# Performance work log

Measured on AMD Instinct MI355X. Metric: run time of the kernel, lower is better.

The kernel has to match this reference:

```python
import jax, jax.numpy as jnp
import numpy as np

B, S, D = 1, 2048, 3072
H, DH = 24, 128
ENC, NIP = 512, 64
COND = (512 // 8) * (512 // 8) * 16 // 64  # 1024 cond tokens per lora
RANK, ALPHA, LW, IP_SCALE = 16, 16.0, 1.0, 1.0
EPS = 1e-5


def _rms(x):
    return x * jax.lax.rsqrt(jnp.mean(x * x, axis=-1, keepdims=True) + EPS)


def _to_heads(x):
    b, s, _ = x.shape
    return x.reshape(b, s, H, DH).transpose(0, 2, 1, 3)  # [B,H,S,DH]


def _from_heads(x):
    b, h, s, d = x.shape
    return x.transpose(0, 2, 1, 3).reshape(b, s, h * d)


def _lora(x, dn, up):
    # token mask keeps only the cond block (number=0, n_loras=1 -> last COND tokens)
    y = ((x[:, -COND:, :] @ dn) @ up) * (ALPHA / RANK)
    z = jnp.zeros((x.shape[0], x.shape[1] - COND, up.shape[1]), x.dtype)
    return jnp.concatenate([z, y], axis=1)


def _sdpa(q, k, v, mask=None):
    s = jnp.einsum('bhqd,bhkd->bhqk', q, k) * (1.0 / np.sqrt(DH))
    if mask is not None:
        s = s + mask
    return jnp.einsum('bhqk,bhkd->bhqd', jax.nn.softmax(s, axis=-1), v)


def _forward(hidden_states, encoder_hidden_states, image_emb,
             Wq, bq, Wk, bk, Wv, bv, Waq, baq, Wak, bak, Wav, bav,
             Wo, bo, Wao, bao, Wkip, Wvip,
             lq_dn, lq_up, lk_dn, lk_up, lv_dn, lv_up, lp_dn, lp_up):
    hs, ehs, img = hidden_states, encoder_hidden_states, image_emb
    # context (encoder) projections + RMSNorm on q/k
    eq = _rms(_to_heads(ehs @ Waq + baq))
    ek = _rms(_to_heads(ehs @ Wak + bak))
    ev = _to_heads(ehs @ Wav + bav)
    # main-stream q/k/v with masked LoRA branches
    q = hs @ Wq + bq + LW * _lora(hs, lq_dn, lq_up)
    k = hs @ Wk + bk + LW * _lora(hs, lk_dn, lk_up)
    v = hs @ Wv + bv + LW * _lora(hs, lv_dn, lv_up)
    q = _rms(_to_heads(q))
    k = _rms(_to_heads(k))
    v = _to_heads(v)
    # IP-adapter branch: extra K/V from image_emb, norm_added_k is RMSNorm(128)
    kip = _rms(_to_heads(img @ Wkip))
    vip = _to_heads(img @ Wvip)
    ip_out = _from_heads(_sdpa(q, kip, vip))  # [B,S,D]
    # concat encoder stream ahead of main stream
    q = jnp.concatenate([eq, q], axis=2)
    k = jnp.concatenate([ek, k], axis=2)
    v = jnp.concatenate([ev, v], axis=2)
    SL = ENC + S
    SB = SL - COND  # scaled_block_size
    m = jnp.ones((SL, SL), jnp.float32)
    m = m.at[:SB, :].set(0.0)        # non-cond rows attend everywhere
    m = m.at[SB:, SB:].set(0.0)      # single cond block attends to itself (n_loras=1)
    mask = m * (-1e20)
    out = _from_heads(_sdpa(q, k, v, mask))  # [B,SL,D]
    enc_out = out[:, :ENC, :]
    main = out[:, ENC:, :] + IP_SCALE * ip_out
    main = main @ Wo + bo
    main = main + LW * _lora(main, lp_dn, lp_up)  # proj LoRA (to_out dropout=identity)
    enc_out = enc_out @ Wao + bao
    return jnp.concatenate([enc_out, main], axis=1)  # [B, ENC+S, D]


def setup_inputs():
    key = jax.random.key(0)
    ks = iter(jax.random.split(key, 40))
    w = lambda *sh: jax.random.normal(next(ks), sh, jnp.float32) * 0.02
    return dict(
        hidden_states=jax.random.normal(next(ks), (B, S, D), jnp.float32),
        encoder_hidden_states=jax.random.normal(next(ks), (B, ENC, D), jnp.float32),
        image_emb=jax.random.normal(next(ks), (B, NIP, D), jnp.float32),
        Wq=w(D, D), bq=w(D), Wk=w(D, D), bk=w(D), Wv=w(D, D), bv=w(D),
        Waq=w(D, D), baq=w(D), Wak=w(D, D), bak=w(D), Wav=w(D, D), bav=w(D),
        Wo=w(D, D), bo=w(D), Wao=w(D, D), bao=w(D),
        Wkip=w(D, D), Wvip=w(D, D),
        lq_dn=w(D, RANK), lq_up=w(RANK, D), lk_dn=w(D, RANK), lk_up=w(RANK, D),
        lv_dn=w(D, RANK), lv_up=w(RANK, D), lp_dn=w(D, RANK), lp_up=w(RANK, D),
    )


def reference(hidden_states, encoder_hidden_states, image_emb,
              Wq, bq, Wk, bk, Wv, bv, Waq, baq, Wak, bak, Wav, bav,
              Wo, bo, Wao, bao, Wkip, Wvip,
              lq_dn, lq_up, lk_dn, lk_up, lv_dn, lv_up, lp_dn, lp_up):
    return _forward(hidden_states, encoder_hidden_states, image_emb,
                    Wq, bq, Wk, bk, Wv, bv, Waq, baq, Wak, bak, Wav, bav,
                    Wo, bo, Wao, bao, Wkip, Wvip,
                    lq_dn, lq_up, lk_dn, lk_up, lv_dn, lv_up, lp_dn, lp_up)
```

## Files before the change

kernel.cpp:

```cpp
#include <hip/hip_runtime.h>

typedef unsigned short u16;
typedef short s16x8 __attribute__((ext_vector_type(8)));
typedef float f32x4 __attribute__((ext_vector_type(4)));
typedef const __attribute__((address_space(1))) unsigned int* as1_u32p;
typedef __attribute__((address_space(3))) unsigned int* as3_u32p;

static_assert(sizeof(s16x8) == 16, "");

struct alignas(8) U16x4 { u16 x, y, z, w; };

__device__ __forceinline__ u16 f2bf(float f) {
  union { float f; unsigned u; } c; c.f = f;
  return (u16)((c.u + 0x7fffu + ((c.u >> 16) & 1u)) >> 16);
}
__device__ __forceinline__ float bf2f(u16 h) {
  union { unsigned u; float f; } c; c.u = ((unsigned)h) << 16;
  return c.f;
}
__device__ __forceinline__ void async16(const void* g, void* l) {
  __builtin_amdgcn_global_load_lds((as1_u32p)g, (as3_u32p)l, 16, 0, 0);
}

__launch_bounds__(256)
__global__ void cvt_bf16(const float* __restrict__ in, u16* __restrict__ out, long n) {
  long i = ((long)blockIdx.x * 256 + threadIdx.x) * 8;
  if (i >= n) return;
  float4 a = *(const float4*)(in + i);
  float4 b = *(const float4*)(in + i + 4);
  U16x4 o0{f2bf(a.x), f2bf(a.y), f2bf(a.z), f2bf(a.w)};
  U16x4 o1{f2bf(b.x), f2bf(b.y), f2bf(b.z), f2bf(b.w)};
  *(U16x4*)(out + i) = o0;
  *(U16x4*)(out + i + 4) = o1;
}

__launch_bounds__(256)
__global__ void cvt_hs(const float* __restrict__ hs, const float* __restrict__ tl,
                       u16* __restrict__ hsb) {
  long idx = (long)blockIdx.x * 256 + threadIdx.x;
  long m = idx / 392, c = idx % 392;
  U16x4 o0, o1;
  if (c < 384) {
    const float* p = hs + m * 3072 + c * 8;
    float4 a = *(const float4*)p;
    float4 b = *(const float4*)(p + 4);
    o0 = U16x4{f2bf(a.x), f2bf(a.y), f2bf(a.z), f2bf(a.w)};
    o1 = U16x4{f2bf(b.x), f2bf(b.y), f2bf(b.z), f2bf(b.w)};
  } else {
    u16 t[8];
#pragma unroll
    for (int i = 0; i < 8; ++i) {
      int r = (int)(c - 384) * 8 + i;
      float v = (m >= 1024 && r < 48) ? tl[(m - 1024) * 48 + r] : 0.f;
      t[i] = f2bf(v);
    }
    o0 = U16x4{t[0], t[1], t[2], t[3]};
    o1 = U16x4{t[4], t[5], t[6], t[7]};
  }
  u16* d = hsb + m * 3136 + c * 8;
  *(U16x4*)d = o0;
  *(U16x4*)(d + 4) = o1;
}

__launch_bounds__(256)
__global__ void pack_bias(const float* __restrict__ a, const float* __restrict__ b,
                          const float* __restrict__ c, float* __restrict__ out) {
  int i = blockIdx.x * 256 + threadIdx.x;
  if (i >= 9216) return;
  out[i] = (i < 3072) ? a[i] : (i < 6144) ? b[i - 3072] : c[i - 6144];
}

struct WTArgs { const float* src[3]; u16* dst[3]; };

__launch_bounds__(256)
__global__ void transpose_w(WTArgs args, int ldd) {
  const float* src = args.src[blockIdx.z];
  u16* dst = args.dst[blockIdx.z];
  __shared__ float tile[32][33];
  int k0 = blockIdx.x * 32, n0 = blockIdx.y * 32;
  int r = threadIdx.x >> 3, c4 = (threadIdx.x & 7) * 4;
  float4 v = *(const float4*)(src + (long)(k0 + r) * 3072 + n0 + c4);
  tile[r][c4 + 0] = v.x; tile[r][c4 + 1] = v.y;
  tile[r][c4 + 2] = v.z; tile[r][c4 + 3] = v.w;
  __syncthreads();
  U16x4 o{f2bf(tile[c4 + 0][r]), f2bf(tile[c4 + 1][r]),
          f2bf(tile[c4 + 2][r]), f2bf(tile[c4 + 3][r])};
  *(U16x4*)(dst + (long)(n0 + r) * ldd + k0 + c4) = o;
}

__launch_bounds__(256)
__global__ void fill_wtail(const float* __restrict__ u0, const float* __restrict__ u1,
                           const float* __restrict__ u2, u16* __restrict__ WTb) {
  int idx = blockIdx.x * 256 + threadIdx.x;
  int n = idx >> 6, i = idx & 63;
  int seg = n / 3072;
  const float* up = (seg == 0) ? u0 : (seg == 1) ? u1 : u2;
  int r = i - seg * 16;
  float v = (r >= 0 && r < 16) ? up[(long)r * 3072 + (n - seg * 3072)] : 0.f;
  WTb[(long)n * 3136 + 3072 + i] = f2bf(v);
}

__launch_bounds__(256)
__global__ void transpose_v(const u16* __restrict__ VB, u16* __restrict__ VT, int T) {
  __shared__ u16 tile[32][34];
  int h = blockIdx.z;
  int t0 = blockIdx.x * 32, d0 = blockIdx.y * 32;
  int r = threadIdx.x >> 3, c4 = (threadIdx.x & 7) * 4;
  U16x4 v = *(const U16x4*)(VB + ((long)h * T + t0 + r) * 128 + d0 + c4);
  tile[r][c4 + 0] = v.x; tile[r][c4 + 1] = v.y;
  tile[r][c4 + 2] = v.z; tile[r][c4 + 3] = v.w;
  __syncthreads();
  U16x4 o{tile[c4 + 0][r], tile[c4 + 1][r], tile[c4 + 2][r], tile[c4 + 3][r]};
  *(U16x4*)(VT + ((long)h * 128 + d0 + r) * T + t0 + c4) = o;
}

__launch_bounds__(256)
__global__ void rms_heads4(const float* __restrict__ in, int col0,
                           u16* __restrict__ out, int do_rms) {
  const int t = blockIdx.x;
  const int w = threadIdx.x >> 6, lane = threadIdx.x & 63;
  const long ps = 64LL * 6144;
#pragma unroll
  for (int hh = 0; hh < 6; ++hh) {
    int h = w * 6 + hh;
    const float* x = in + (long)t * 6144 + col0 + h * 128 + lane * 2;
    float a = x[0] + x[ps] + x[2 * ps] + x[3 * ps];
    float b = x[1] + x[1 + ps] + x[1 + 2 * ps] + x[1 + 3 * ps];
    float scale = 1.f;
    if (do_rms) {
      float ss = a * a + b * b;
#pragma unroll
      for (int st = 1; st < 64; st <<= 1) ss += __shfl_xor(ss, st, 64);
      scale = rsqrtf(ss * (1.f / 128.f) + 1e-5f);
    }
    unsigned pa = f2bf(a * scale), pb = f2bf(b * scale);
    *(unsigned*)(out + ((long)h * 64 + t) * 128 + lane * 2) = pa | (pb << 16);
  }
}

__launch_bounds__(256)
__global__ void lora_dn3(const float* __restrict__ X, int ldx,
                         const float* __restrict__ d0, const float* __restrict__ d1,
                         const float* __restrict__ d2, float* __restrict__ t) {
  __shared__ float red[4][48];
  const int m = blockIdx.x;
  const float* xr = X + (long)m * ldx;
  float p[48];
#pragma unroll
  for (int r = 0; r < 48; ++r) p[r] = 0.f;
  for (int k = threadIdx.x; k < 3072; k += 256) {
    float a = xr[k];
    const float* e0 = d0 + (long)k * 16;
    const float* e1 = d1 + (long)k * 16;
    const float* e2 = d2 + (long)k * 16;
#pragma unroll
    for (int r = 0; r < 16; ++r) {
      p[r]      += a * e0[r];
      p[16 + r] += a * e1[r];
      p[32 + r] += a * e2[r];
    }
  }
#pragma unroll
  for (int r = 0; r < 48; ++r)
#pragma unroll
    for (int st = 1; st < 64; st <<= 1) p[r] += __shfl_xor(p[r], st, 64);
  int lane = threadIdx.x & 63, w = threadIdx.x >> 6;
  if (lane == 0) {
#pragma unroll
    for (int r = 0; r < 48; ++r) red[w][r] = p[r];
  }
  __syncthreads();
  if (threadIdx.x < 48) {
    int r = threadIdx.x;
    t[(long)m * 48 + r] = red[0][r] + red[1][r] + red[2][r] + red[3][r];
  }
}

__launch_bounds__(256)
__global__ void lora_dn(const float* __restrict__ X, int ldx,
                        const float* __restrict__ dn, float* __restrict__ t) {
  __shared__ float red[4][16];
  const int m = blockIdx.x;
  const float* xr = X + (long)m * ldx;
  float p[16];
#pragma unroll
  for (int r = 0; r < 16; ++r) p[r] = 0.f;
  for (int k = threadIdx.x; k < 3072; k += 256) {
    float a = xr[k];
    const float* d = dn + (long)k * 16;
#pragma unroll
    for (int r = 0; r < 16; ++r) p[r] += a * d[r];
  }
#pragma unroll
  for (int r = 0; r < 16; ++r)
#pragma unroll
    for (int st = 1; st < 64; st <<= 1) p[r] += __shfl_xor(p[r], st, 64);
  int lane = threadIdx.x & 63, w = threadIdx.x >> 6;
  if (lane == 0) {
#pragma unroll
    for (int r = 0; r < 16; ++r) red[w][r] = p[r];
  }
  __syncthreads();
  if (threadIdx.x < 16) {
    int r = threadIdx.x;
    t[(long)m * 16 + r] = red[0][r] + red[1][r] + red[2][r] + red[3][r];
  }
}

__launch_bounds__(256)
__global__ void lora_up(const float* __restrict__ t, const float* __restrict__ up,
                        float* __restrict__ Y, int ldy) {
  const int m = blockIdx.x;
  float tv[16];
#pragma unroll
  for (int r = 0; r < 16; ++r) tv[r] = t[(long)m * 16 + r];
  float* yr = Y + (long)m * ldy;
  for (int n = threadIdx.x; n < 3072; n += 256) {
    float a = 0.f;
#pragma unroll
    for (int r = 0; r < 16; ++r) a += tv[r] * up[(long)r * 3072 + n];
    yr[n] += a;
  }
}

template <int BM, int MI, int NI>
__launch_bounds__(256)
__global__ void gemm_f32(const u16* __restrict__ A, int lda,
                         const u16* __restrict__ B, int ldb,
                         float* __restrict__ C, int ldc,
                         const float* __restrict__ bias, int KC, long cstride) {
  constexpr int WCOLS = 128 / (NI * 16);
  constexpr int ABYTES = BM * 128;
  __shared__ char smem[ABYTES + 128 * 128];
  char* As = smem;
  char* Bs = smem + ABYTES;
  const int tid = threadIdx.x;
  const int w = tid >> 6, lane = tid & 63;
  const int lr = lane & 15, lg = lane >> 4;
  const int wr = w / WCOLS, wc = w % WCOLS;
  const int nbx = gridDim.x;
  const int nwg = nbx * gridDim.y;
  const int flat = blockIdx.y * nbx + blockIdx.x;
  const int swz = (flat & 7) * (nwg >> 3) + (flat >> 3);
  const long m0 = (long)(swz % nbx) * BM;
  const long n0 = (long)(swz / nbx) * 128;
  const int k0 = blockIdx.z * KC;
  C += blockIdx.z * cstride;
  f32x4 acc[MI][NI] = {};
  constexpr int ACH = BM / 32;
  for (int kb = k0; kb < k0 + KC; kb += 64) {
    __syncthreads();
#pragma unroll
    for (int i = 0; i < ACH; ++i) {
      int x = (tid + 256 * i) * 16;
      int row = x >> 7;
      int sx = x ^ ((row & 7) << 4);
      async16((const char*)(A + (m0 + row) * lda + kb) + (sx & 127),
              As + ((w << 10) + (i << 12)));
    }
#pragma unroll
    for (int i = 0; i < 4; ++i) {
      int x = (tid + 256 * i) * 16;
      int row = x >> 7;
      int sx = x ^ ((row & 7) << 4);
      async16((const char*)(B + (n0 + row) * ldb + kb) + (sx & 127),
              Bs + ((w << 10) + (i << 12)));
    }
    __syncthreads();
#pragma unroll
    for (int kc = 0; kc < 2; ++kc) {
      s16x8 af[MI], bfr[NI];
#pragma unroll
      for (int mi = 0; mi < MI; ++mi) {
        int row = wr * (MI * 16) + mi * 16 + lr;
        int b = ((row << 7) + kc * 64 + lg * 16) ^ ((row & 7) << 4);
        af[mi] = *(const s16x8*)(As + b);
      }
#pragma unroll
      for (int ni = 0; ni < NI; ++ni) {
        int row = wc * (NI * 16) + ni * 16 + lr;
        int b = ((row << 7) + kc * 64 + lg * 16) ^ ((row & 7) << 4);
        bfr[ni] = *(const s16x8*)(Bs + b);
      }
#pragma unroll
      for (int mi = 0; mi < MI; ++mi)
#pragma unroll
        for (int ni = 0; ni < NI; ++ni)
          acc[mi][ni] = __builtin_amdgcn_mfma_f32_16x16x32_bf16(af[mi], bfr[ni], acc[mi][ni], 0, 0, 0);
    }
  }
#pragma unroll
  for (int mi = 0; mi < MI; ++mi) {
#pragma unroll
    for (int ni = 0; ni < NI; ++ni) {
      long col = n0 + wc * (NI * 16) + ni * 16 + lr;
      float bv = bias ? bias[col] : 0.f;
#pragma unroll
      for (int j = 0; j < 4; ++j) {
        long row = m0 + wr * (MI * 16) + mi * 16 + lg * 4 + j;
        C[row * ldc + col] = acc[mi][ni][j] + bv;
      }
    }
  }
}

__launch_bounds__(256)
__global__ void gemm_qkv(const u16* __restrict__ A, int lda,
                         const u16* __restrict__ B, int ldb,
                         u16* __restrict__ Qo, u16* __restrict__ Ko, u16* __restrict__ VTo,
                         int t0, const float* __restrict__ bias, int K) {
  __shared__ char smem[128 * 128 + 128 * 128];
  char* As = smem;
  char* Bs = smem + 128 * 128;
  const int tid = threadIdx.x;
  const int w = tid >> 6, lane = tid & 63;
  const int lr = lane & 15, lg = lane >> 4;
  const int wr = w >> 1, wc = w & 1;
  const int nbx = gridDim.x;
  const int nwg = nbx * gridDim.y;
  const int flat = blockIdx.y * nbx + blockIdx.x;
  const int swz = (flat & 7) * (nwg >> 3) + (flat >> 3);
  const long m0 = (long)(swz % nbx) * 128;
  const long n0 = (long)(swz / nbx) * 128;
  f32x4 acc[4][4] = {};
  for (int kb = 0; kb < K; kb += 64) {
    __syncthreads();
#pragma unroll
    for (int i = 0; i < 4; ++i) {
      int x = (tid + 256 * i) * 16;
      int row = x >> 7;
      int sx = x ^ ((row & 7) << 4);
      async16((const char*)(A + (m0 + row) * lda + kb) + (sx & 127),
              As + ((w << 10) + (i << 12)));
    }
#pragma unroll
    for (int i = 0; i < 4; ++i) {
      int x = (tid + 256 * i) * 16;
      int row = x >> 7;
      int sx = x ^ ((row & 7) << 4);
      async16((const char*)(B + (n0 + row) * ldb + kb) + (sx & 127),
              Bs + ((w << 10) + (i << 12)));
    }
    __syncthreads();
#pragma unroll
    for (int kc = 0; kc < 2; ++kc) {
      s16x8 af[4], bfr[4];
#pragma unroll
      for (int mi = 0; mi < 4; ++mi) {
        int row = wr * 64 + mi * 16 + lr;
        int b = ((row << 7) + kc * 64 + lg * 16) ^ ((row & 7) << 4);
        af[mi] = *(const s16x8*)(As + b);
      }
#pragma unroll
      for (int ni = 0; ni < 4; ++ni) {
        int row = wc * 64 + ni * 16 + lr;
        int b = ((row << 7) + kc * 64 + lg * 16) ^ ((row & 7) << 4);
        bfr[ni] = *(const s16x8*)(Bs + b);
      }
#pragma unroll
      for (int mi = 0; mi < 4; ++mi)
#pragma unroll
        for (int ni = 0; ni < 4; ++ni)
          acc[mi][ni] = __builtin_amdgcn_mfma_f32_16x16x32_bf16(af[mi], bfr[ni], acc[mi][ni], 0, 0, 0);
    }
  }
  const int seg = (int)(n0 / 3072);
  const int head = (int)((n0 % 3072) >> 7);
#pragma unroll
  for (int ni = 0; ni < 4; ++ni) {
    float bv = bias[n0 + wc * 64 + ni * 16 + lr];
#pragma unroll
    for (int mi = 0; mi < 4; ++mi)
#pragma unroll
      for (int j = 0; j < 4; ++j) acc[mi][ni][j] += bv;
  }
  if (seg < 2) {
    u16* out = (seg == 0) ? Qo : Ko;
    float scl[4][4];
#pragma unroll
    for (int mi = 0; mi < 4; ++mi)
#pragma unroll
      for (int j = 0; j < 4; ++j) {
        float s = 0.f;
#pragma unroll
        for (int ni = 0; ni < 4; ++ni) s += acc[mi][ni][j] * acc[mi][ni][j];
#pragma unroll
        for (int st = 1; st < 16; st <<= 1) s += __shfl_xor(s, st, 16);
        scl[mi][j] = s;
      }
    __syncthreads();
    float* red = (float*)smem;
    if (lr == 0) {
#pragma unroll
      for (int mi = 0; mi < 4; ++mi)
#pragma unroll
        for (int j = 0; j < 4; ++j)
          red[((((wr * 4 + mi) * 4 + lg) * 4 + j) << 1) + wc] = scl[mi][j];
    }
    __syncthreads();
#pragma unroll
    for (int mi = 0; mi < 4; ++mi)
#pragma unroll
      for (int j = 0; j < 4; ++j) {
        int ix = (((wr * 4 + mi) * 4 + lg) * 4 + j) << 1;
        float t = red[ix] + red[ix + 1];
        scl[mi][j] = rsqrtf(t * (1.f / 128.f) + 1e-5f);
      }
#pragma unroll
    for (int mi = 0; mi < 4; ++mi)
#pragma unroll
      for (int ni = 0; ni < 4; ++ni) {
        int d = wc * 64 + ni * 16 + lr;
#pragma unroll
        for (int j = 0; j < 4; ++j) {
          long tok = t0 + m0 + wr * 64 + mi * 16 + lg * 4 + j;
          out[((long)head * 2560 + tok) * 128 + d] = f2bf(acc[mi][ni][j] * scl[mi][j]);
        }
      }
  } else {
#pragma unroll
    for (int mi = 0; mi < 4; ++mi)
#pragma unroll
      for (int ni = 0; ni < 4; ++ni) {
        long tok0 = t0 + m0 + wr * 64 + mi * 16 + lg * 4;
        int d = wc * 64 + ni * 16 + lr;
        U16x4 o{f2bf(acc[mi][ni][0]), f2bf(acc[mi][ni][1]),
                f2bf(acc[mi][ni][2]), f2bf(acc[mi][ni][3])};
        *(U16x4*)(VTo + ((long)head * 128 + d) * 2560 + tok0) = o;
      }
  }
}

__launch_bounds__(256)
__global__ void gemm_out(const u16* __restrict__ Atok, const u16* __restrict__ WT,
                         float* __restrict__ outp, const float* __restrict__ bao,
                         const float* __restrict__ bo) {
  __shared__ char smem[128 * 128 + 128 * 128];
  char* As = smem;
  char* Bs = smem + 128 * 128;
  const int tid = threadIdx.x;
  const int w = tid >> 6, lane = tid & 63;
  const int lr = lane & 15, lg = lane >> 4;
  const int wr = w >> 1, wc = w & 1;
  const int flat = blockIdx.y * 20 + blockIdx.x;
  const int swz = (flat & 7) * 60 + (flat >> 3);
  const int mx = swz % 20;
  const long n0 = (long)(swz / 20) * 128;
  const u16* A;
  const u16* B;
  const float* bias;
  float* C;
  long m0;
  if (mx < 4) { A = Atok; B = WT; bias = bao; C = outp; m0 = (long)mx * 128; }
  else { A = Atok + 512L * 3072; B = WT + 3072L * 3136; bias = bo; C = outp + 512L * 3072; m0 = (long)(mx - 4) * 128; }
  f32x4 acc[4][4] = {};
  for (int kb = 0; kb < 3072; kb += 64) {
    __syncthreads();
#pragma unroll
    for (int i = 0; i < 4; ++i) {
      int x = (tid + 256 * i) * 16;
      int row = x >> 7;
      int sx = x ^ ((row & 7) << 4);
      async16((const char*)(A + (m0 + row) * 3072 + kb) + (sx & 127),
              As + ((w << 10) + (i << 12)));
    }
#pragma unroll
    for (int i = 0; i < 4; ++i) {
      int x = (tid + 256 * i) * 16;
      int row = x >> 7;
      int sx = x ^ ((row & 7) << 4);
      async16((const char*)(B + (n0 + row) * 3136 + kb) + (sx & 127),
              Bs + ((w << 10) + (i << 12)));
    }
    __syncthreads();
#pragma unroll
    for (int kc = 0; kc < 2; ++kc) {
      s16x8 af[4], bfr[4];
#pragma unroll
      for (int mi = 0; mi < 4; ++mi) {
        int row = wr * 64 + mi * 16 + lr;
        int b = ((row << 7) + kc * 64 + lg * 16) ^ ((row & 7) << 4);
        af[mi] = *(const s16x8*)(As + b);
      }
#pragma unroll
      for (int ni = 0; ni < 4; ++ni) {
        int row = wc * 64 + ni * 16 + lr;
        int b = ((row << 7) + kc * 64 + lg * 16) ^ ((row & 7) << 4);
        bfr[ni] = *(const s16x8*)(Bs + b);
      }
#pragma unroll
      for (int mi = 0; mi < 4; ++mi)
#pragma unroll
        for (int ni = 0; ni < 4; ++ni)
          acc[mi][ni] = __builtin_amdgcn_mfma_f32_16x16x32_bf16(af[mi], bfr[ni], acc[mi][ni], 0, 0, 0);
    }
  }
#pragma unroll
  for (int mi = 0; mi < 4; ++mi) {
#pragma unroll
    for (int ni = 0; ni < 4; ++ni) {
      long col = n0 + wc * 64 + ni * 16 + lr;
      float bv = bias[col];
#pragma unroll
      for (int j = 0; j < 4; ++j) {
        long row = m0 + wr * 64 + mi * 16 + lg * 4 + j;
        C[row * 3072 + col] = acc[mi][ni][j] + bv;
      }
    }
  }
}

__launch_bounds__(512, 4)
__global__ void attn_fused(const u16* __restrict__ QB, const u16* __restrict__ KB,
                           const u16* __restrict__ VT, const u16* __restrict__ KipB,
                           const u16* __restrict__ VipT, u16* __restrict__ OutTok) {
  __shared__ char smem[81920];
  const int tid = threadIdx.x, w = tid >> 6, lane = tid & 63;
  const int lr = lane & 15, lg = lane >> 4;
  const int h = blockIdx.y;
  const int q0 = blockIdx.x * 128;
  const bool ip = (q0 >= 512);
  const u16* Qrow = QB + (long)(h * 2560 + q0 + w * 16 + lr) * 128;
  s16x8 qf[4];
#pragma unroll
  for (int dc = 0; dc < 4; ++dc) qf[dc] = *(const s16x8*)(Qrow + dc * 32 + lg * 8);
  f32x4 accO[8] = {};
  float l_r[4] = {0.f, 0.f, 0.f, 0.f};
  const int kv0 = (q0 >= 1536) ? 1536 : 0;
  const float sc = 0.08838834764831845f;

  auto stage_main = [&](int kv, int buf) {
#pragma unroll
    for (int i = 0; i < 2; ++i) {
      int x = (tid + 512 * i) * 16;
      int row = x >> 8;
      int sx = x ^ ((row & 7) << 4);
      async16((const char*)(KB + (long)(h * 2560 + kv + row) * 128) + (sx & 255),
              smem + buf * 16384 + ((i << 13) + (w << 10)));
    }
#pragma unroll
    for (int i = 0; i < 2; ++i) {
      int x = (tid + 512 * i) * 16;
      int row = x >> 7;
      int sx = x ^ ((row & 7) << 4);
      async16((const char*)(VT + (long)(h * 128 + row) * 2560 + kv) + (sx & 127),
              smem + 32768 + buf * 16384 + ((i << 13) + (w << 10)));
    }
  };
  auto stage_ip = [&](int buf) {
#pragma unroll
    for (int i = 0; i < 2; ++i) {
      int x = (tid + 512 * i) * 16;
      int row = x >> 8;
      int sx = x ^ ((row & 7) << 4);
      async16((const char*)(KipB + (long)(h * 64 + row) * 128) + (sx & 255),
              smem + buf * 16384 + ((i << 13) + (w << 10)));
    }
#pragma unroll
    for (int i = 0; i < 2; ++i) {
      int x = (tid + 512 * i) * 16;
      int row = x >> 7;
      int sx = x ^ ((row & 7) << 4);
      async16((const char*)(VipT + (long)(h * 128 + row) * 64) + (sx & 127),
              smem + 32768 + buf * 16384 + ((i << 13) + (w << 10)));
    }
  };

  stage_main(kv0, 0);
  __syncthreads();
  int cur = 0;
  for (int kv = kv0; kv < 2560; kv += 64) {
    if (kv + 64 < 2560) stage_main(kv + 64, cur ^ 1);
    else if (ip) stage_ip(cur ^ 1);
    const char* Ks = smem + cur * 16384;
    const char* Vs = smem + 32768 + cur * 16384;
    char* Pw = smem + 65536 + w * 2048;
    f32x4 s[4] = {};
#pragma unroll
    for (int kt = 0; kt < 4; ++kt)
#pragma unroll
      for (int dc = 0; dc < 4; ++dc) {
        int row = kt * 16 + lr;
        int b = ((row << 8) + dc * 64 + lg * 16) ^ ((row & 7) << 4);
        s16x8 kf = *(const s16x8*)(Ks + b);
        s[kt] = __builtin_amdgcn_mfma_f32_16x16x32_bf16(qf[dc], kf, s[kt], 0, 0, 0);
      }
#pragma unroll
    for (int kt = 0; kt < 4; ++kt)
#pragma unroll
      for (int j = 0; j < 4; ++j) {
        float pv = __expf(fmaf(s[kt][j], sc, -12.0f));
        l_r[j] += pv;
        int prow = lg * 4 + j;
        int b = ((prow << 7) + (kt * 16 + lr) * 2) ^ ((prow & 7) << 4);
        *(u16*)(Pw + b) = f2bf(pv);
      }
    asm volatile("s_waitcnt lgkmcnt(0)" ::: "memory");
#pragma unroll
    for (int kc = 0; kc < 2; ++kc) {
      int pb = ((lr << 7) + kc * 64 + lg * 16) ^ ((lr & 7) << 4);
      s16x8 pf = *(const s16x8*)(Pw + pb);
#pragma unroll
      for (int dt = 0; dt < 8; ++dt) {
        int row = dt * 16 + lr;
        int b = ((row << 7) + kc * 64 + lg * 16) ^ ((row & 7) << 4);
        s16x8 vf = *(const s16x8*)(Vs + b);
        accO[dt] = __builtin_amdgcn_mfma_f32_16x16x32_bf16(pf, vf, accO[dt], 0, 0, 0);
      }
    }
    __syncthreads();
    cur ^= 1;
  }
#pragma unroll
  for (int j = 0; j < 4; ++j) {
#pragma unroll
    for (int st = 1; st < 16; st <<= 1) l_r[j] += __shfl_xor(l_r[j], st, 16);
    l_r[j] = 1.f / l_r[j];
  }
#pragma unroll
  for (int dt = 0; dt < 8; ++dt)
#pragma unroll
    for (int j = 0; j < 4; ++j) accO[dt][j] *= l_r[j];
  if (ip) {
    const char* Ks = smem + cur * 16384;
    const char* Vs = smem + 32768 + cur * 16384;
    char* Pw = smem + 65536 + w * 2048;
    f32x4 s2[4] = {};
#pragma unroll
    for (int kt = 0; kt < 4; ++kt)
#pragma unroll
      for (int dc = 0; dc < 4; ++dc) {
        int row = kt * 16 + lr;
        int b = ((row << 8) + dc * 64 + lg * 16) ^ ((row & 7) << 4);
        s16x8 kf = *(const s16x8*)(Ks + b);
        s2[kt] = __builtin_amdgcn_mfma_f32_16x16x32_bf16(qf[dc], kf, s2[kt], 0, 0, 0);
      }
    float p2[4][4];
    float l2[4] = {0.f, 0.f, 0.f, 0.f};
#pragma unroll
    for (int kt = 0; kt < 4; ++kt)
#pragma unroll
      for (int j = 0; j < 4; ++j) {
        float pv = __expf(fmaf(s2[kt][j], sc, -12.0f));
        p2[kt][j] = pv;
        l2[j] += pv;
      }
#pragma unroll
    for (int j = 0; j < 4; ++j) {
#pragma unroll
      for (int st = 1; st < 16; st <<= 1) l2[j] += __shfl_xor(l2[j], st, 16);
      l2[j] = 1.f / l2[j];
    }
#pragma unroll
    for (int kt = 0; kt < 4; ++kt)
#pragma unroll
      for (int j = 0; j < 4; ++j) {
        int prow = lg * 4 + j;
        int b = ((prow << 7) + (kt * 16 + lr) * 2) ^ ((prow & 7) << 4);
        *(u16*)(Pw + b) = f2bf(p2[kt][j] * l2[j]);
      }
    asm volatile("s_waitcnt lgkmcnt(0)" ::: "memory");
#pragma unroll
    for (int kc = 0; kc < 2; ++kc) {
      int pb = ((lr << 7) + kc * 64 + lg * 16) ^ ((lr & 7) << 4);
      s16x8 pf = *(const s16x8*)(Pw + pb);
#pragma unroll
      for (int dt = 0; dt < 8; ++dt) {
        int row = dt * 16 + lr;
        int b = ((row << 7) + kc * 64 + lg * 16) ^ ((row & 7) << 4);
        s16x8 vf = *(const s16x8*)(Vs + b);
        accO[dt] = __builtin_amdgcn_mfma_f32_16x16x32_bf16(pf, vf, accO[dt], 0, 0, 0);
      }
    }
  }
#pragma unroll
  for (int j = 0; j < 4; ++j) {
    long tok = q0 + w * 16 + lg * 4 + j;
#pragma unroll
    for (int dt = 0; dt < 8; ++dt) {
      long col = h * 128 + dt * 16 + lr;
      OutTok[tok * 3072 + col] = f2bf(accO[dt][j]);
    }
  }
}


extern "C" void kernel_launch(void* const* d_in, const int* in_sizes, int n_in,
                              void* d_out, int out_size, void* d_ws, size_t ws_size,
                              hipStream_t stream) {
  const float* hs    = (const float*)d_in[0];
  const float* ehs   = (const float*)d_in[1];
  const float* img   = (const float*)d_in[2];
  const float* Wq    = (const float*)d_in[3];
  const float* bq    = (const float*)d_in[4];
  const float* Wk    = (const float*)d_in[5];
  const float* bk    = (const float*)d_in[6];
  const float* Wv    = (const float*)d_in[7];
  const float* bv    = (const float*)d_in[8];
  const float* Waq   = (const float*)d_in[9];
  const float* baq   = (const float*)d_in[10];
  const float* Wak   = (const float*)d_in[11];
  const float* bak   = (const float*)d_in[12];
  const float* Wav   = (const float*)d_in[13];
  const float* bav   = (const float*)d_in[14];
  const float* Wo    = (const float*)d_in[15];
  const float* bo    = (const float*)d_in[16];
  const float* Wao   = (const float*)d_in[17];
  const float* bao   = (const float*)d_in[18];
  const float* Wkip  = (const float*)d_in[19];
  const float* Wvip  = (const float*)d_in[20];
  const float* lq_dn = (const float*)d_in[21];
  const float* lq_up = (const float*)d_in[22];
  const float* lk_dn = (const float*)d_in[23];
  const float* lk_up = (const float*)d_in[24];
  const float* lv_dn = (const float*)d_in[25];
  const float* lv_up = (const float*)d_in[26];
  const float* lp_dn = (const float*)d_in[27];
  const float* lp_up = (const float*)d_in[28];
  float* outp = (float*)d_out;

  char* ws = (char*)d_ws;
  size_t off = 0;
  auto take = [&](size_t b) { char* p = ws + off; off += (b + 255) & ~(size_t)255; return p; };
  u16*   WTb  = (u16*)take(9216LL * 3136 * 2);
  u16*   hsb  = (u16*)take(2048LL * 3136 * 2);
  u16*   ehsb = (u16*)take(512LL * 3072 * 2);
  u16*   imgb = (u16*)take(64LL * 3072 * 2);
  u16*   QBf  = (u16*)take(24LL * 2560 * 128 * 2);
  u16*   KBf  = (u16*)take(24LL * 2560 * 128 * 2);
  u16*   VTf  = (u16*)take(24LL * 128 * 2560 * 2);
  u16*   AttnTok = (u16*)take(2560LL * 3072 * 2);
  float* IP0  = (float*)take(4LL * 64 * 6144 * 4);
  u16*   KipB = (u16*)take(24LL * 64 * 128 * 2);
  u16*   VipB = (u16*)take(24LL * 64 * 128 * 2);
  u16*   VipT = (u16*)take(24LL * 128 * 64 * 2);
  float* bpk  = (float*)take(9216 * 4);
  float* tl   = (float*)take(1024LL * 48 * 4);

  lora_dn3<<<1024, 256, 0, stream>>>(hs + 1024LL * 3072, 3072, lq_dn, lk_dn, lv_dn, tl);
  cvt_hs<<<3136, 256, 0, stream>>>(hs, tl, hsb);
  cvt_bf16<<<768, 256, 0, stream>>>(ehs, ehsb, 512LL * 3072);
  cvt_bf16<<<96, 256, 0, stream>>>(img, imgb, 64LL * 3072);

  pack_bias<<<36, 256, 0, stream>>>(baq, bak, bav, bpk);
  {
    WTArgs a;
    a.src[0] = Waq; a.dst[0] = WTb;
    a.src[1] = Wak; a.dst[1] = WTb + 3072LL * 3136;
    a.src[2] = Wav; a.dst[2] = WTb + 2 * 3072LL * 3136;
    transpose_w<<<dim3(96, 96, 3), 256, 0, stream>>>(a, 3136);
  }
  gemm_qkv<<<dim3(4, 72), 256, 0, stream>>>(ehsb, 3072, WTb, 3136, QBf, KBf, VTf, 0, bpk, 3072);

  {
    WTArgs a;
    a.src[0] = Wkip; a.dst[0] = WTb;
    a.src[1] = Wvip; a.dst[1] = WTb + 3072LL * 3136;
    a.src[2] = Wkip; a.dst[2] = WTb;
    transpose_w<<<dim3(96, 96, 2), 256, 0, stream>>>(a, 3136);
  }
  gemm_f32<64, 4, 2><<<dim3(1, 48, 4), 256, 0, stream>>>(imgb, 3072, WTb, 3136, IP0, 6144,
                                                          nullptr, 768, 64LL * 6144);
  rms_heads4<<<64, 256, 0, stream>>>(IP0, 0, KipB, 1);
  rms_heads4<<<64, 256, 0, stream>>>(IP0, 3072, VipB, 0);
  transpose_v<<<dim3(2, 4, 24), 256, 0, stream>>>(VipB, VipT, 64);

  pack_bias<<<36, 256, 0, stream>>>(bq, bk, bv, bpk);
  {
    WTArgs a;
    a.src[0] = Wq; a.dst[0] = WTb;
    a.src[1] = Wk; a.dst[1] = WTb + 3072LL * 3136;
    a.src[2] = Wv; a.dst[2] = WTb + 2 * 3072LL * 3136;
    transpose_w<<<dim3(96, 96, 3), 256, 0, stream>>>(a, 3136);
  }
  fill_wtail<<<2304, 256, 0, stream>>>(lq_up, lk_up, lv_up, WTb);
  gemm_qkv<<<dim3(16, 72), 256, 0, stream>>>(hsb, 3136, WTb, 3136, QBf, KBf, VTf, 512, bpk, 3136);

  attn_fused<<<dim3(20, 24), 512, 0, stream>>>(QBf, KBf, VTf, KipB, VipT, AttnTok);

  {
    WTArgs a;
    a.src[0] = Wao; a.dst[0] = WTb;
    a.src[1] = Wo;  a.dst[1] = WTb + 3072LL * 3136;
    a.src[2] = Wao; a.dst[2] = WTb;
    transpose_w<<<dim3(96, 96, 2), 256, 0, stream>>>(a, 3136);
  }
  gemm_out<<<dim3(20, 24), 256, 0, stream>>>(AttnTok, WTb, outp, bao, bo);

  lora_dn<<<1024, 256, 0, stream>>>(outp + 1536LL * 3072, 3072, lp_dn, tl);
  lora_up<<<1024, 256, 0, stream>>>(tl, lp_up, outp + 1536LL * 3072, 3072);
}
```

Measured before the change: 670.3 us.

## Widen QKV GEMM tile to 128x256 with LDS-staged coalesced epilogue

The fused QKV projection GEMM now computes 128x256 output tiles, so each warp covers one full head width (128 dims) and the per-row RMSNorm reduction happens within the warp instead of through a shared-memory cross-warp reduction. The epilogue stages each head's bf16 output through swizzled LDS and writes it with 16-byte coalesced stores, rather than scattered 2-byte and 8-byte stores. The grid is halved to match the wider tiles. This raises A-tile reuse and store efficiency, at the cost of twice the accumulator registers, more LDS, and fewer workgroups per launch.

```diff
diff --git a/kernel.cpp b/kernel.cpp
--- a/kernel.cpp
+++ b/kernel.cpp
@@ -304,14 +304,14 @@
   }
 }
 
-__launch_bounds__(256)
+__launch_bounds__(256, 2)
 __global__ void gemm_qkv(const u16* __restrict__ A, int lda,
                          const u16* __restrict__ B, int ldb,
                          u16* __restrict__ Qo, u16* __restrict__ Ko, u16* __restrict__ VTo,
                          int t0, const float* __restrict__ bias, int K) {
-  __shared__ char smem[128 * 128 + 128 * 128];
+  __shared__ char smem[49152];
   char* As = smem;
-  char* Bs = smem + 128 * 128;
+  char* Bs = smem + 16384;
   const int tid = threadIdx.x;
   const int w = tid >> 6, lane = tid & 63;
   const int lr = lane & 15, lg = lane >> 4;
@@ -321,113 +321,114 @@
   const int flat = blockIdx.y * nbx + blockIdx.x;
   const int swz = (flat & 7) * (nwg >> 3) + (flat >> 3);
   const long m0 = (long)(swz % nbx) * 128;
-  const long n0 = (long)(swz / nbx) * 128;
-  f32x4 acc[4][4] = {};
+  const long n0 = (long)(swz / nbx) * 256;
+  f32x4 acc[4][8] = {};
   for (int kb = 0; kb < K; kb += 64) {
     __syncthreads();
 #pragma unroll
     for (int i = 0; i < 4; ++i) {
       int x = (tid + 256 * i) * 16;
       int row = x >> 7;
-      int sx = x ^ ((row & 7) << 4);
-      async16((const char*)(A + (m0 + row) * lda + kb) + (sx & 127),
-              As + ((w << 10) + (i << 12)));
-    }
-#pragma unroll
-    for (int i = 0; i < 4; ++i) {
+      int sx = (x & 127) ^ ((row & 7) << 4);
+      async16((const char*)(A + (m0 + row) * lda + kb) + sx, As + x);
+    }
+#pragma unroll
+    for (int i = 0; i < 8; ++i) {
       int x = (tid + 256 * i) * 16;
       int row = x >> 7;
-      int sx = x ^ ((row & 7) << 4);
-      async16((const char*)(B + (n0 + row) * ldb + kb) + (sx & 127),
-              Bs + ((w << 10) + (i << 12)));
+      int sx = (x & 127) ^ ((row & 7) << 4);
+      async16((const char*)(B + (n0 + row) * ldb + kb) + sx, Bs + x);
     }
     __syncthreads();
 #pragma unroll
     for (int kc = 0; kc < 2; ++kc) {
-      s16x8 af[4], bfr[4];
+      s16x8 af[4], bfr[8];
 #pragma unroll
       for (int mi = 0; mi < 4; ++mi) {
         int row = wr * 64 + mi * 16 + lr;
-        int b = ((row << 7) + kc * 64 + lg * 16) ^ ((row & 7) << 4);
-        af[mi] = *(const s16x8*)(As + b);
-      }
-#pragma unroll
-      for (int ni = 0; ni < 4; ++ni) {
-        int row = wc * 64 + ni * 16 + lr;
-        int b = ((row << 7) + kc * 64 + lg * 16) ^ ((row & 7) << 4);
-        bfr[ni] = *(const s16x8*)(Bs + b);
+        af[mi] = *(const s16x8*)(As + (row << 7) + ((kc * 64 + lg * 16) ^ ((row & 7) << 4)));
+      }
+#pragma unroll
+      for (int ni = 0; ni < 8; ++ni) {
+        int row = wc * 128 + ni * 16 + lr;
+        bfr[ni] = *(const s16x8*)(Bs + (row << 7) + ((kc * 64 + lg * 16) ^ ((row & 7) << 4)));
       }
 #pragma unroll
       for (int mi = 0; mi < 4; ++mi)
 #pragma unroll
-        for (int ni = 0; ni < 4; ++ni)
+        for (int ni = 0; ni < 8; ++ni)
           acc[mi][ni] = __builtin_amdgcn_mfma_f32_16x16x32_bf16(af[mi], bfr[ni], acc[mi][ni], 0, 0, 0);
     }
   }
   const int seg = (int)(n0 / 3072);
-  const int head = (int)((n0 % 3072) >> 7);
-#pragma unroll
-  for (int ni = 0; ni < 4; ++ni) {
-    float bv = bias[n0 + wc * 64 + ni * 16 + lr];
+  const int head0 = (int)((n0 % 3072) >> 7);
+#pragma unroll
+  for (int ni = 0; ni < 8; ++ni) {
+    float bv = bias[n0 + wc * 128 + ni * 16 + lr];
 #pragma unroll
     for (int mi = 0; mi < 4; ++mi)
 #pragma unroll
       for (int j = 0; j < 4; ++j) acc[mi][ni][j] += bv;
   }
+  float scl[4][4];
   if (seg < 2) {
-    u16* out = (seg == 0) ? Qo : Ko;
-    float scl[4][4];
 #pragma unroll
     for (int mi = 0; mi < 4; ++mi)
 #pragma unroll
       for (int j = 0; j < 4; ++j) {
         float s = 0.f;
 #pragma unroll
-        for (int ni = 0; ni < 4; ++ni) s += acc[mi][ni][j] * acc[mi][ni][j];
+        for (int ni = 0; ni < 8; ++ni) s += acc[mi][ni][j] * acc[mi][ni][j];
 #pragma unroll
         for (int st = 1; st < 16; st <<= 1) s += __shfl_xor(s, st, 16);
-        scl[mi][j] = s;
-      }
-    __syncthreads();
-    float* red = (float*)smem;
-    if (lr == 0) {
-#pragma unroll
-      for (int mi = 0; mi < 4; ++mi)
-#pragma unroll
-        for (int j = 0; j < 4; ++j)
-          red[((((wr * 4 + mi) * 4 + lg) * 4 + j) << 1) + wc] = scl[mi][j];
-    }
-    __syncthreads();
-#pragma unroll
-    for (int mi = 0; mi < 4; ++mi)
-#pragma unroll
-      for (int j = 0; j < 4; ++j) {
-        int ix = (((wr * 4 + mi) * 4 + lg) * 4 + j) << 1;
-        float t = red[ix] + red[ix + 1];
-        scl[mi][j] = rsqrtf(t * (1.f / 128.f) + 1e-5f);
-      }
-#pragma unroll
-    for (int mi = 0; mi < 4; ++mi)
-#pragma unroll
-      for (int ni = 0; ni < 4; ++ni) {
-        int d = wc * 64 + ni * 16 + lr;
-#pragma unroll
-        for (int j = 0; j < 4; ++j) {
-          long tok = t0 + m0 + wr * 64 + mi * 16 + lg * 4 + j;
-          out[((long)head * 2560 + tok) * 128 + d] = f2bf(acc[mi][ni][j] * scl[mi][j]);
-        }
-      }
-  } else {
-#pragma unroll
-    for (int mi = 0; mi < 4; ++mi)
-#pragma unroll
-      for (int ni = 0; ni < 4; ++ni) {
-        long tok0 = t0 + m0 + wr * 64 + mi * 16 + lg * 4;
-        int d = wc * 64 + ni * 16 + lr;
-        U16x4 o{f2bf(acc[mi][ni][0]), f2bf(acc[mi][ni][1]),
-                f2bf(acc[mi][ni][2]), f2bf(acc[mi][ni][3])};
-        *(U16x4*)(VTo + ((long)head * 128 + d) * 2560 + tok0) = o;
-      }
+        scl[mi][j] = rsqrtf(s * (1.f / 128.f) + 1e-5f);
+      }
+  }
+#pragma unroll
+  for (int ph = 0; ph < 2; ++ph) {
+    __syncthreads();
+    if (wc == ph) {
+      if (seg < 2) {
+#pragma unroll
+        for (int mi = 0; mi < 4; ++mi)
+#pragma unroll
+          for (int ni = 0; ni < 8; ++ni) {
+            int d2 = (ni * 16 + lr) * 2;
+#pragma unroll
+            for (int j = 0; j < 4; ++j) {
+              int tok = wr * 64 + mi * 16 + lg * 4 + j;
+              *(u16*)(smem + tok * 256 + (d2 ^ ((tok & 7) << 4))) =
+                  f2bf(acc[mi][ni][j] * scl[mi][j]);
+            }
+          }
+      } else {
+#pragma unroll
+        for (int mi = 0; mi < 4; ++mi)
+#pragma unroll
+          for (int ni = 0; ni < 8; ++ni) {
+            int d = ni * 16 + lr;
+            int tok0b = (wr * 64 + mi * 16 + lg * 4) * 2;
+            U16x4 o{f2bf(acc[mi][ni][0]), f2bf(acc[mi][ni][1]),
+                    f2bf(acc[mi][ni][2]), f2bf(acc[mi][ni][3])};
+            *(U16x4*)(smem + d * 256 + (tok0b ^ ((d & 7) << 4))) = o;
+          }
+      }
+    }
+    __syncthreads();
+    const int headp = head0 + ph;
+#pragma unroll
+    for (int i = 0; i < 8; ++i) {
+      int x = (tid + 256 * i) * 16;
+      int row = x >> 8, col = x & 255;
+      s16x8 vdat = *(const s16x8*)(smem + row * 256 + (col ^ ((row & 7) << 4)));
+      if (seg < 2) {
+        u16* g = (seg == 0 ? Qo : Ko) + ((long)headp * 2560 + t0 + m0 + row) * 128;
+        *(s16x8*)((char*)g + col) = vdat;
+      } else {
+        u16* g = VTo + ((long)headp * 128 + row) * 2560 + t0 + m0;
+        *(s16x8*)((char*)g + col) = vdat;
+      }
+    }
   }
 }
 
@@ -750,7 +751,7 @@
     a.src[2] = Wav; a.dst[2] = WTb + 2 * 3072LL * 3136;
     transpose_w<<<dim3(96, 96, 3), 256, 0, stream>>>(a, 3136);
   }
-  gemm_qkv<<<dim3(4, 72), 256, 0, stream>>>(ehsb, 3072, WTb, 3136, QBf, KBf, VTf, 0, bpk, 3072);
+  gemm_qkv<<<dim3(4, 36), 256, 0, stream>>>(ehsb, 3072, WTb, 3136, QBf, KBf, VTf, 0, bpk, 3072);
 
   {
     WTArgs a;
@@ -774,7 +775,7 @@
     transpose_w<<<dim3(96, 96, 3), 256, 0, stream>>>(a, 3136);
   }
   fill_wtail<<<2304, 256, 0, stream>>>(lq_up, lk_up, lv_up, WTb);
-  gemm_qkv<<<dim3(16, 72), 256, 0, stream>>>(hsb, 3136, WTb, 3136, QBf, KBf, VTf, 512, bpk, 3136);
+  gemm_qkv<<<dim3(16, 36), 256, 0, stream>>>(hsb, 3136, WTb, 3136, QBf, KBf, VTf, 512, bpk, 3136);
 
   attn_fused<<<dim3(20, 24), 512, 0, stream>>>(QBf, KBf, VTf, KipB, VipT, AttnTok);
 
```

New measurement: 668.5 us. Within noise of the previous version (-0.3%).
